# Kernel optimization log

Hardware: AMD Instinct MI355X
Metric: run time of the kernel (lower is better)

Reference implementation:

```python
import jax, jax.numpy as jnp
import numpy as np

N_HEAD = 16
ROT_DIM = 64  # head_dim * rotary_percentage(1.0)
ROPE_BASE = 10000.0
NEG_INF = -1.0e9


def _rope_cos_sin(seq_len, rd):
    # freqs: [S, rd//2]; original code builds cos/sin per pair; we repeat each
    # entry twice so it applies to the interleaved (even, odd) pair layout.
    inv_freq = 1.0 / (ROPE_BASE ** (jnp.arange(0, rd, 2, dtype=jnp.float32) / rd))
    freqs = jnp.arange(seq_len, dtype=jnp.float32)[:, None] * inv_freq[None, :]
    cos = jnp.repeat(jnp.cos(freqs), 2, axis=-1)  # [S, rd]
    sin = jnp.repeat(jnp.sin(freqs), 2, axis=-1)  # [S, rd]
    return cos, sin


def _rotate_pairs(x):
    # interleaved pairs: (x0, x1) -> (-x1, x0), matching apply_rotary_embeddings
    x2 = x.reshape(x.shape[:-1] + (-1, 2))
    r = jnp.stack([-x2[..., 1], x2[..., 0]], axis=-1)
    return r.reshape(x.shape)


def reference(x, W_attn, W_proj, cache_k, cache_v):
    B, S, D = x.shape
    H = N_HEAD
    HD = D // H
    # fused QKV projection (Linear, bias=False)
    qkv = x @ W_attn  # [B, S, 3D]
    q, k, v = jnp.split(qkv, 3, axis=-1)
    q = q.reshape(B, S, H, HD).transpose(0, 2, 1, 3)  # [B,H,S,HD]
    k = k.reshape(B, S, H, HD).transpose(0, 2, 1, 3)
    v = v.reshape(B, S, H, HD).transpose(0, 2, 1, 3)
    # rotary on first ROT_DIM dims; q = q*cos - rot(q)*sin (original sign conv.)
    cos, sin = _rope_cos_sin(S, ROT_DIM)  # [S, ROT_DIM] broadcasts over B,H
    q_r, q_p = q[..., :ROT_DIM], q[..., ROT_DIM:]
    k_r, k_p = k[..., :ROT_DIM], k[..., ROT_DIM:]
    q_r = q_r * cos - _rotate_pairs(q_r) * sin
    k_r = k_r * cos - _rotate_pairs(k_r) * sin
    q = jnp.concatenate([q_r, q_p], axis=-1)
    k = jnp.concatenate([k_r, k_p], axis=-1)
    # KV-cache write at past_length=0 (prefill), then read back full context
    k_full = jax.lax.dynamic_update_slice(cache_k, k, (0, 0, 0, 0))
    v_full = jax.lax.dynamic_update_slice(cache_v, v, (0, 0, 0, 0))
    T = k_full.shape[2]  # full_seq_len == S here
    # causal additive mask (upper triangular * -1e9), as in the kv_cache branch
    mask = jnp.triu(jnp.ones((T, T), dtype=jnp.float32), k=1) * NEG_INF
    q = q * (1.0 / np.sqrt(HD).astype(np.float32))
    scores = jnp.einsum('bhqd,bhkd->bhqk', q, k_full) + mask
    att = jax.nn.softmax(scores, axis=-1)
    y = jnp.einsum('bhqk,bhkd->bhqd', att, v_full)
    y = y.transpose(0, 2, 1, 3).reshape(B, S, D)
    return y @ W_proj


def setup_inputs() -> dict:
    key = jax.random.key(0)
    k1, k2, k3 = jax.random.split(key, 3)
    B, S, D, H = 2, 2048, 1024, 16
    HD = D // H
    x = jax.random.normal(k1, (B, S, D), dtype=jnp.float32)
    W_attn = jax.random.normal(k2, (D, 3 * D), dtype=jnp.float32) * 0.02
    W_proj = jax.random.normal(k3, (D, D), dtype=jnp.float32) * 0.02
    cache_k = jnp.zeros((B, H, S, HD), dtype=jnp.float32)
    cache_v = jnp.zeros((B, H, S, HD), dtype=jnp.float32)
    return {"x": x, "W_attn": W_attn, "W_proj": W_proj, "cache_k": cache_k, "cache_v": cache_v}
```

## Files before the change

### kernel.cpp

```cpp
#include <hip/hip_runtime.h>
#include <stdint.h>

#define S_LEN 2048
#define NHEAD 16
#define DMODEL 1024

typedef __attribute__((ext_vector_type(8))) short short8;
typedef __attribute__((ext_vector_type(8))) __bf16 bf16x8;
typedef __attribute__((ext_vector_type(4))) float f32x4;

__device__ __forceinline__ unsigned short f2b(float f) {
  unsigned int u = __float_as_uint(f);
  u += 0x7fffu + ((u >> 16) & 1u);
  return (unsigned short)(u >> 16);
}
__device__ __forceinline__ float b2f(unsigned short h) {
  return __uint_as_float(((unsigned int)h) << 16);
}
__device__ __forceinline__ f32x4 mfma16(short8 a, short8 b, f32x4 c) {
  return __builtin_amdgcn_mfma_f32_16x16x32_bf16(
      __builtin_bit_cast(bf16x8, a), __builtin_bit_cast(bf16x8, b), c, 0, 0, 0);
}
__device__ __forceinline__ void gload16(const void* g, void* l) {
  __builtin_amdgcn_global_load_lds(
      (const __attribute__((address_space(1))) unsigned int*)g,
      (__attribute__((address_space(3))) unsigned int*)l, 16, 0, 0);
}

__global__ __launch_bounds__(256) void cast_f32_bf16(
    const float* __restrict__ in, unsigned short* __restrict__ out, long n) {
  long i = ((long)blockIdx.x * 256 + threadIdx.x) * 4;
  if (i >= n) return;
  float4 v = *(const float4*)(in + i);
  ushort4 o;
  o.x = f2b(v.x); o.y = f2b(v.y); o.z = f2b(v.z); o.w = f2b(v.w);
  *(ushort4*)(out + i) = o;
}

__global__ __launch_bounds__(256) void transpose_cast(
    const float* __restrict__ W, unsigned short* __restrict__ Wt, int K, int N) {
  __shared__ float t[32][33];
  const int nt = blockIdx.x, kt = blockIdx.y;
  const int tx = threadIdx.x, ty = threadIdx.y;
#pragma unroll
  for (int j = 0; j < 4; ++j)
    t[ty + j * 8][tx] = W[(long)(kt * 32 + ty + j * 8) * N + nt * 32 + tx];
  __syncthreads();
#pragma unroll
  for (int j = 0; j < 4; ++j)
    Wt[(long)(nt * 32 + ty + j * 8) * K + kt * 32 + tx] = f2b(t[tx][ty + j * 8]);
}

__global__ __launch_bounds__(256) void make_tab(float2* __restrict__ tab) {
  int i = blockIdx.x * 256 + threadIdx.x;
  if (i >= S_LEN * 32) return;
  int s = i >> 5, fi = i & 31;
  float inv = powf(10000.0f, -(float)(2 * fi) / 64.0f);
  float fr = (float)s * inv;
  tab[i] = make_float2(cosf(fr), sinf(fr));
}

template <int OUT_BF16>
__global__ __launch_bounds__(256) void gemm_bt(
    const unsigned short* __restrict__ A, const unsigned short* __restrict__ Bt,
    void* __restrict__ Cout, int M, int N, int K) {
  __shared__ __align__(16) unsigned short As[128 * 32];
  __shared__ __align__(16) unsigned short Bs[128 * 32];
  const int tid = threadIdx.x;
  const int wave = tid >> 6, lane = tid & 63;
  const int g = lane >> 4, r15 = lane & 15;
  const int wm = wave >> 1, wn = wave & 1;
  const long m0 = (long)blockIdx.x * 128, n0 = (long)blockIdx.y * 128;
  const int srow = tid >> 2, scol = (tid & 3) * 8;
  const unsigned short* Ag = A + (m0 + srow) * K + scol;
  const unsigned short* Bg = Bt + (n0 + srow) * K + scol;
  unsigned short* As0 = &As[srow * 32 + scol];
  unsigned short* As1 = &As[(srow + 64) * 32 + scol];
  unsigned short* Bs0 = &Bs[srow * 32 + scol];
  unsigned short* Bs1 = &Bs[(srow + 64) * 32 + scol];
  f32x4 acc[4][4] = {};
  for (int kt = 0; kt < K; kt += 32) {
    __syncthreads();
    gload16(Ag + kt, As0);
    gload16(Ag + (long)64 * K + kt, As1);
    gload16(Bg + kt, Bs0);
    gload16(Bg + (long)64 * K + kt, Bs1);
    __syncthreads();
    short8 a[4], b[4];
#pragma unroll
    for (int m = 0; m < 4; ++m)
      a[m] = *(const short8*)&As[(wm * 64 + m * 16 + r15) * 32 + g * 8];
#pragma unroll
    for (int n = 0; n < 4; ++n)
      b[n] = *(const short8*)&Bs[(wn * 64 + n * 16 + r15) * 32 + g * 8];
#pragma unroll
    for (int m = 0; m < 4; ++m)
#pragma unroll
      for (int n = 0; n < 4; ++n)
        acc[m][n] = mfma16(a[m], b[n], acc[m][n]);
  }
#pragma unroll
  for (int m = 0; m < 4; ++m)
#pragma unroll
    for (int n = 0; n < 4; ++n)
#pragma unroll
      for (int r = 0; r < 4; ++r) {
        long row = m0 + wm * 64 + m * 16 + g * 4 + r;
        long col = n0 + wn * 64 + n * 16 + r15;
        if (OUT_BF16)
          ((unsigned short*)Cout)[row * N + col] = f2b(acc[m][n][r]);
        else
          ((float*)Cout)[row * N + col] = acc[m][n][r];
      }
}

__global__ __launch_bounds__(256) void rope_scatter(
    const unsigned short* __restrict__ qkv, const float2* __restrict__ tab,
    unsigned short* __restrict__ Qb, unsigned short* __restrict__ Kb) {
  long p = (long)blockIdx.x * 256 + threadIdx.x;
  if (p >= (long)4096 * 1024) return;
  int row = (int)(p >> 10);
  int col = ((int)(p & 1023)) * 2;
  int seg = col >> 10;
  int cc = col & 1023;
  int h = cc >> 6, d = cc & 63;
  int b = row >> 11, s = row & 2047;
  const unsigned short* src = qkv + (long)row * 3072 + col;
  float v0 = b2f(src[0]), v1 = b2f(src[1]);
  float2 f = tab[s * 32 + (d >> 1)];
  float o0 = v0 * f.x + v1 * f.y;
  float o1 = v1 * f.x - v0 * f.y;
  float scl = seg ? 1.0f : 0.125f;
  unsigned short* dst = (seg ? Kb : Qb) + (((long)(b * NHEAD + h) * S_LEN + s) * 64 + d);
  dst[0] = f2b(o0 * scl);
  dst[1] = f2b(o1 * scl);
}

__global__ __launch_bounds__(256) void v_transpose(
    const unsigned short* __restrict__ qkv, unsigned short* __restrict__ Vt) {
  __shared__ unsigned short t[64][33];
  const int st = blockIdx.x;
  const int dt = blockIdx.y;
  const int bh = blockIdx.z;
  const int b = bh >> 4, h = bh & 15;
  const int tx = threadIdx.x, ty = threadIdx.y;
#pragma unroll
  for (int j = 0; j < 8; ++j)
    t[ty + j * 8][tx] =
        qkv[((long)b * S_LEN + st * 64 + ty + j * 8) * 3072 + 2048 + h * 64 + dt * 32 + tx];
  __syncthreads();
#pragma unroll
  for (int j = 0; j < 4; ++j) {
    const int d_local = ty + j * 8;
#pragma unroll
    for (int jj = 0; jj < 2; ++jj) {
      const int col = jj * 32 + tx;
      const int kv = (col & 3) * 16 + (col >> 2);
      Vt[((long)bh * 64 + dt * 32 + d_local) * S_LEN + st * 64 + col] = t[kv][d_local];
    }
  }
}

__device__ __forceinline__ void load_k(const unsigned short* __restrict__ Kp,
                                       int kpos, int c, int g, short8 kf[4][2]) {
#pragma unroll
  for (int s = 0; s < 4; ++s)
#pragma unroll
    for (int hh = 0; hh < 2; ++hh)
      kf[s][hh] = *(const short8*)(Kp + (long)(kpos + s * 16 + c) * 64 + hh * 32 + g * 8);
}
__device__ __forceinline__ void load_v(const unsigned short* __restrict__ Vp,
                                       int kpos, int c, int g, short8 vf[4][2]) {
#pragma unroll
  for (int dt = 0; dt < 4; ++dt)
#pragma unroll
    for (int hh = 0; hh < 2; ++hh)
      vf[dt][hh] = *(const short8*)(Vp + (long)(dt * 16 + c) * S_LEN + kpos + hh * 32 + g * 8);
}

template <bool MASKED, bool PREFETCH>
__device__ __forceinline__ void attn_tile(
    int kpos0, int qbase, int c, int g,
    const short8& q0, const short8& q1,
    short8 kf[4][2], short8 vf[4][2],
    f32x4 O[4], float mrow[4], float lrow[4],
    unsigned char* PwB,
    const unsigned short* __restrict__ Kp, const unsigned short* __restrict__ Vp) {
  f32x4 s[4];
#pragma unroll
  for (int sub = 0; sub < 4; ++sub) {
    f32x4 z = {};
    z = mfma16(q0, kf[sub][0], z);
    s[sub] = mfma16(q1, kf[sub][1], z);
  }
  if (PREFETCH) load_k(Kp, kpos0 + 64, c, g, kf);
  float sc[4];
#pragma unroll
  for (int r = 0; r < 4; ++r) {
    float a0 = s[0][r], a1 = s[1][r], a2 = s[2][r], a3 = s[3][r];
    if (MASKED) {
      const int q = qbase + g * 4 + r;
      a0 = (kpos0 + c <= q) ? a0 : -1e30f;
      a1 = (kpos0 + 16 + c <= q) ? a1 : -1e30f;
      a2 = (kpos0 + 32 + c <= q) ? a2 : -1e30f;
      a3 = (kpos0 + 48 + c <= q) ? a3 : -1e30f;
    }
    float mt = fmaxf(fmaxf(a0, a1), fmaxf(a2, a3));
    mt = fmaxf(mt, __shfl_xor(mt, 1));
    mt = fmaxf(mt, __shfl_xor(mt, 2));
    mt = fmaxf(mt, __shfl_xor(mt, 4));
    mt = fmaxf(mt, __shfl_xor(mt, 8));
    const float mnew = fmaxf(mrow[r], mt);
    sc[r] = __expf(mrow[r] - mnew);
    mrow[r] = mnew;
    a0 = __expf(a0 - mnew);
    a1 = __expf(a1 - mnew);
    a2 = __expf(a2 - mnew);
    a3 = __expf(a3 - mnew);
    float rs = (a0 + a1) + (a2 + a3);
    rs += __shfl_xor(rs, 1);
    rs += __shfl_xor(rs, 2);
    rs += __shfl_xor(rs, 4);
    rs += __shfl_xor(rs, 8);
    lrow[r] = lrow[r] * sc[r] + rs;
    unsigned int lo, hi;
    asm("v_cvt_pk_bf16_f32 %0, %1, %2" : "=v"(lo) : "v"(a0), "v"(a1));
    asm("v_cvt_pk_bf16_f32 %0, %1, %2" : "=v"(hi) : "v"(a2), "v"(a3));
    const int qr = g * 4 + r;
    *(uint2*)(PwB + qr * 128 + ((c * 8) ^ ((qr & 7) << 4))) = make_uint2(lo, hi);
  }
#pragma unroll
  for (int dt = 0; dt < 4; ++dt) {
    f32x4 o = O[dt];
    o[0] *= sc[0]; o[1] *= sc[1]; o[2] *= sc[2]; o[3] *= sc[3];
    O[dt] = o;
  }
  __builtin_amdgcn_wave_barrier();
  const int rb = c * 128, swz = (c & 7) << 4;
  const short8 pa0 = *(const short8*)(PwB + rb + ((g * 16) ^ swz));
  const short8 pa1 = *(const short8*)(PwB + rb + ((64 + g * 16) ^ swz));
#pragma unroll
  for (int dt = 0; dt < 4; ++dt) {
    O[dt] = mfma16(pa0, vf[dt][0], O[dt]);
    O[dt] = mfma16(pa1, vf[dt][1], O[dt]);
  }
  __builtin_amdgcn_wave_barrier();
  if (PREFETCH) load_v(Vp, kpos0 + 64, c, g, vf);
}

__global__ __launch_bounds__(64) void attn_v3(
    const unsigned short* __restrict__ Qb, const unsigned short* __restrict__ Kb,
    const unsigned short* __restrict__ Vt, unsigned short* __restrict__ yb) {
  __shared__ __align__(16) unsigned char PwB[2048];
  const int flat = (int)blockIdx.x + ((int)blockIdx.y << 7);
  const int xcd = flat & 7;
  const int rest = flat >> 3;
  const int bh = xcd * 4 + (rest >> 7);
  const int p = 127 - (rest & 127);
  const int lane = (int)threadIdx.x & 63;
  const int g = lane >> 4, c = lane & 15;
  const int b = bh >> 4, h = bh & 15;
  const unsigned short* Kp = Kb + (long)bh * (S_LEN * 64);
  const unsigned short* Vp = Vt + (long)bh * (64 * S_LEN);
  short8 kf[4][2], vf[4][2];

  const int qbase = p << 4;
  const unsigned short* Qp = Qb + ((long)bh * S_LEN + qbase) * 64;
  const short8 q0 = *(const short8*)(Qp + c * 64 + g * 8);
  const short8 q1 = *(const short8*)(Qp + c * 64 + 32 + g * 8);
  f32x4 O[4] = {};
  float mrow[4] = {-1e30f, -1e30f, -1e30f, -1e30f};
  float lrow[4] = {0.f, 0.f, 0.f, 0.f};
  const int nfull = qbase >> 6;

  load_k(Kp, 0, c, g, kf);
  load_v(Vp, 0, c, g, vf);
  for (int t = 0; t < nfull; ++t)
    attn_tile<false, true>(t * 64, qbase, c, g, q0, q1, kf, vf, O, mrow, lrow, PwB, Kp, Vp);
  attn_tile<true, false>(nfull * 64, qbase, c, g, q0, q1, kf, vf, O, mrow, lrow, PwB, Kp, Vp);

  float inv[4];
#pragma unroll
  for (int r = 0; r < 4; ++r) inv[r] = 1.0f / lrow[r];
#pragma unroll
  for (int dt = 0; dt < 4; ++dt)
#pragma unroll
    for (int r = 0; r < 4; ++r) {
      long row = (long)b * S_LEN + qbase + g * 4 + r;
      yb[row * DMODEL + h * 64 + dt * 16 + c] = f2b(O[dt][r] * inv[r]);
    }
}

extern "C" void kernel_launch(void* const* d_in, const int* in_sizes, int n_in,
                              void* d_out, int out_size, void* d_ws, size_t ws_size,
                              hipStream_t stream) {
  const float* x = (const float*)d_in[0];
  const float* Wa = (const float*)d_in[1];
  const float* Wp = (const float*)d_in[2];
  float* out = (float*)d_out;

  char* ws = (char*)d_ws;
  size_t off = 0;
  auto alloc = [&](size_t bytes) -> void* {
    off = (off + 255) & ~(size_t)255;
    void* p = ws + off;
    off += bytes;
    return p;
  };
  unsigned short* xb   = (unsigned short*)alloc((size_t)4096 * 1024 * 2);
  unsigned short* WaT  = (unsigned short*)alloc((size_t)3072 * 1024 * 2);
  unsigned short* WpT  = (unsigned short*)alloc((size_t)1024 * 1024 * 2);
  unsigned short* qkvb = (unsigned short*)alloc((size_t)4096 * 3072 * 2);
  float2* tab          = (float2*)alloc((size_t)2048 * 32 * sizeof(float2));
  unsigned short* Qb   = (unsigned short*)alloc((size_t)32 * 2048 * 64 * 2);
  unsigned short* Kb   = (unsigned short*)alloc((size_t)32 * 2048 * 64 * 2);
  unsigned short* Vt   = (unsigned short*)alloc((size_t)32 * 2048 * 64 * 2);
  unsigned short* yb   = xb;

  dim3 tB(32, 8);
  cast_f32_bf16<<<4096, 256, 0, stream>>>(x, xb, (long)4096 * 1024);
  transpose_cast<<<dim3(96, 32), tB, 0, stream>>>(Wa, WaT, 1024, 3072);
  transpose_cast<<<dim3(32, 32), tB, 0, stream>>>(Wp, WpT, 1024, 1024);
  make_tab<<<256, 256, 0, stream>>>(tab);
  gemm_bt<1><<<dim3(32, 24), 256, 0, stream>>>(xb, WaT, (void*)qkvb, 4096, 3072, 1024);
  rope_scatter<<<16384, 256, 0, stream>>>(qkvb, tab, Qb, Kb);
  v_transpose<<<dim3(32, 2, 32), tB, 0, stream>>>(qkvb, Vt);
  attn_v3<<<dim3(128, 32), 64, 0, stream>>>(Qb, Kb, Vt, yb);
  gemm_bt<0><<<dim3(32, 8), 256, 0, stream>>>(yb, WpT, (void*)out, 4096, 1024, 1024);
}
```

Baseline: 317.0 us.

## Switch attention to 32x32x16 MFMA with transposed scores and register-only P

Rewrites the attention kernel to use 32x32x16 bf16 MFMA, computing S^T = K·Q^T so each lane owns one query row. Softmax row reductions then need only a single cross-half shuffle. P is passed to the PV MFMA through lane shuffles instead of a shared-memory round trip. Each wave now handles 32 queries instead of 16, so the grid halves and K/V loads are reused across more rows. The V transpose drops its interleaved permutation to match the new layout. The cost is a larger per-thread register footprint and fewer, heavier waves.

Measured after the change: 277.2 us. 1.14x faster.

```diff
diff --git a/kernel.cpp b/kernel.cpp
--- a/kernel.cpp
+++ b/kernel.cpp
@@ -8,6 +8,7 @@
 typedef __attribute__((ext_vector_type(8))) short short8;
 typedef __attribute__((ext_vector_type(8))) __bf16 bf16x8;
 typedef __attribute__((ext_vector_type(4))) float f32x4;
+typedef __attribute__((ext_vector_type(16))) float f32x16;
 
 __device__ __forceinline__ unsigned short f2b(float f) {
   unsigned int u = __float_as_uint(f);
@@ -20,6 +21,15 @@
 __device__ __forceinline__ f32x4 mfma16(short8 a, short8 b, f32x4 c) {
   return __builtin_amdgcn_mfma_f32_16x16x32_bf16(
       __builtin_bit_cast(bf16x8, a), __builtin_bit_cast(bf16x8, b), c, 0, 0, 0);
+}
+__device__ __forceinline__ f32x16 mfma32(short8 a, short8 b, f32x16 c) {
+  return __builtin_amdgcn_mfma_f32_32x32x16_bf16(
+      __builtin_bit_cast(bf16x8, a), __builtin_bit_cast(bf16x8, b), c, 0, 0, 0);
+}
+__device__ __forceinline__ unsigned int cvtpk(float lo, float hi) {
+  unsigned int r;
+  asm("v_cvt_pk_bf16_f32 %0, %1, %2" : "=v"(r) : "v"(lo), "v"(hi));
+  return r;
 }
 __device__ __forceinline__ void gload16(const void* g, void* l) {
   __builtin_amdgcn_global_load_lds(
@@ -155,139 +165,141 @@
 #pragma unroll
     for (int jj = 0; jj < 2; ++jj) {
       const int col = jj * 32 + tx;
-      const int kv = (col & 3) * 16 + (col >> 2);
-      Vt[((long)bh * 64 + dt * 32 + d_local) * S_LEN + st * 64 + col] = t[kv][d_local];
+      Vt[((long)bh * 64 + dt * 32 + d_local) * S_LEN + st * 64 + col] = t[col][d_local];
     }
   }
 }
 
-__device__ __forceinline__ void load_k(const unsigned short* __restrict__ Kp,
-                                       int kpos, int c, int g, short8 kf[4][2]) {
-#pragma unroll
-  for (int s = 0; s < 4; ++s)
-#pragma unroll
-    for (int hh = 0; hh < 2; ++hh)
-      kf[s][hh] = *(const short8*)(Kp + (long)(kpos + s * 16 + c) * 64 + hh * 32 + g * 8);
-}
-__device__ __forceinline__ void load_v(const unsigned short* __restrict__ Vp,
-                                       int kpos, int c, int g, short8 vf[4][2]) {
-#pragma unroll
-  for (int dt = 0; dt < 4; ++dt)
-#pragma unroll
-    for (int hh = 0; hh < 2; ++hh)
-      vf[dt][hh] = *(const short8*)(Vp + (long)(dt * 16 + c) * S_LEN + kpos + hh * 32 + g * 8);
+__device__ __forceinline__ void load_k32(const unsigned short* __restrict__ Kp,
+                                         int kv0, int q31, int hi, short8 kf[2][4]) {
+#pragma unroll
+  for (int sub = 0; sub < 2; ++sub)
+#pragma unroll
+    for (int dc = 0; dc < 4; ++dc)
+      kf[sub][dc] = *(const short8*)(Kp + (long)(kv0 + sub * 32 + q31) * 64 + dc * 16 + hi * 8);
+}
+__device__ __forceinline__ void load_v32(const unsigned short* __restrict__ Vp,
+                                         int kv0, int q31, int hi, short8 vf[2][4]) {
+#pragma unroll
+  for (int dv = 0; dv < 2; ++dv)
+#pragma unroll
+    for (int c = 0; c < 4; ++c)
+      vf[dv][c] = *(const short8*)(Vp + (long)(dv * 32 + q31) * S_LEN + kv0 + c * 16 + hi * 8);
 }
 
 template <bool MASKED, bool PREFETCH>
-__device__ __forceinline__ void attn_tile(
-    int kpos0, int qbase, int c, int g,
-    const short8& q0, const short8& q1,
-    short8 kf[4][2], short8 vf[4][2],
-    f32x4 O[4], float mrow[4], float lrow[4],
-    unsigned char* PwB,
+__device__ __forceinline__ void attn_tile32(
+    int kv0, int qbase, int q31, int hi,
+    const short8 qf[4], short8 kf[2][4], short8 vf[2][4],
+    f32x16& o0, f32x16& o1, float& m, float& l,
     const unsigned short* __restrict__ Kp, const unsigned short* __restrict__ Vp) {
-  f32x4 s[4];
-#pragma unroll
-  for (int sub = 0; sub < 4; ++sub) {
-    f32x4 z = {};
-    z = mfma16(q0, kf[sub][0], z);
-    s[sub] = mfma16(q1, kf[sub][1], z);
-  }
-  if (PREFETCH) load_k(Kp, kpos0 + 64, c, g, kf);
-  float sc[4];
-#pragma unroll
-  for (int r = 0; r < 4; ++r) {
-    float a0 = s[0][r], a1 = s[1][r], a2 = s[2][r], a3 = s[3][r];
-    if (MASKED) {
-      const int q = qbase + g * 4 + r;
-      a0 = (kpos0 + c <= q) ? a0 : -1e30f;
-      a1 = (kpos0 + 16 + c <= q) ? a1 : -1e30f;
-      a2 = (kpos0 + 32 + c <= q) ? a2 : -1e30f;
-      a3 = (kpos0 + 48 + c <= q) ? a3 : -1e30f;
+  f32x16 s0 = {}, s1 = {};
+#pragma unroll
+  for (int dc = 0; dc < 4; ++dc) s0 = mfma32(kf[0][dc], qf[dc], s0);
+#pragma unroll
+  for (int dc = 0; dc < 4; ++dc) s1 = mfma32(kf[1][dc], qf[dc], s1);
+  if (PREFETCH) load_k32(Kp, kv0 + 64, q31, hi, kf);
+  if (MASKED) {
+    const int q = qbase + q31;
+#pragma unroll
+    for (int i = 0; i < 16; ++i) {
+      const int rel = (i & 3) + 8 * (i >> 2) + 4 * hi;
+      s0[i] = (kv0 + rel <= q) ? s0[i] : -1e30f;
+      s1[i] = (kv0 + 32 + rel <= q) ? s1[i] : -1e30f;
     }
-    float mt = fmaxf(fmaxf(a0, a1), fmaxf(a2, a3));
-    mt = fmaxf(mt, __shfl_xor(mt, 1));
-    mt = fmaxf(mt, __shfl_xor(mt, 2));
-    mt = fmaxf(mt, __shfl_xor(mt, 4));
-    mt = fmaxf(mt, __shfl_xor(mt, 8));
-    const float mnew = fmaxf(mrow[r], mt);
-    sc[r] = __expf(mrow[r] - mnew);
-    mrow[r] = mnew;
-    a0 = __expf(a0 - mnew);
-    a1 = __expf(a1 - mnew);
-    a2 = __expf(a2 - mnew);
-    a3 = __expf(a3 - mnew);
-    float rs = (a0 + a1) + (a2 + a3);
-    rs += __shfl_xor(rs, 1);
-    rs += __shfl_xor(rs, 2);
-    rs += __shfl_xor(rs, 4);
-    rs += __shfl_xor(rs, 8);
-    lrow[r] = lrow[r] * sc[r] + rs;
-    unsigned int lo, hi;
-    asm("v_cvt_pk_bf16_f32 %0, %1, %2" : "=v"(lo) : "v"(a0), "v"(a1));
-    asm("v_cvt_pk_bf16_f32 %0, %1, %2" : "=v"(hi) : "v"(a2), "v"(a3));
-    const int qr = g * 4 + r;
-    *(uint2*)(PwB + qr * 128 + ((c * 8) ^ ((qr & 7) << 4))) = make_uint2(lo, hi);
-  }
-#pragma unroll
-  for (int dt = 0; dt < 4; ++dt) {
-    f32x4 o = O[dt];
-    o[0] *= sc[0]; o[1] *= sc[1]; o[2] *= sc[2]; o[3] *= sc[3];
-    O[dt] = o;
-  }
-  __builtin_amdgcn_wave_barrier();
-  const int rb = c * 128, swz = (c & 7) << 4;
-  const short8 pa0 = *(const short8*)(PwB + rb + ((g * 16) ^ swz));
-  const short8 pa1 = *(const short8*)(PwB + rb + ((64 + g * 16) ^ swz));
-#pragma unroll
-  for (int dt = 0; dt < 4; ++dt) {
-    O[dt] = mfma16(pa0, vf[dt][0], O[dt]);
-    O[dt] = mfma16(pa1, vf[dt][1], O[dt]);
-  }
-  __builtin_amdgcn_wave_barrier();
-  if (PREFETCH) load_v(Vp, kpos0 + 64, c, g, vf);
-}
-
-__global__ __launch_bounds__(64) void attn_v3(
+  }
+  float t8[8];
+#pragma unroll
+  for (int i = 0; i < 8; ++i)
+    t8[i] = fmaxf(fmaxf(s0[2 * i], s0[2 * i + 1]), fmaxf(s1[2 * i], s1[2 * i + 1]));
+  float mt = fmaxf(fmaxf(fmaxf(t8[0], t8[1]), fmaxf(t8[2], t8[3])),
+                   fmaxf(fmaxf(t8[4], t8[5]), fmaxf(t8[6], t8[7])));
+  mt = fmaxf(mt, __shfl_xor(mt, 32));
+  const float mnew = fmaxf(m, mt);
+  const float scl = __expf(m - mnew);
+  m = mnew;
+#pragma unroll
+  for (int i = 0; i < 16; ++i) {
+    s0[i] = __expf(s0[i] - mnew);
+    s1[i] = __expf(s1[i] - mnew);
+  }
+  float a8[8];
+#pragma unroll
+  for (int i = 0; i < 8; ++i)
+    a8[i] = (s0[2 * i] + s0[2 * i + 1]) + (s1[2 * i] + s1[2 * i + 1]);
+  float rs = ((a8[0] + a8[1]) + (a8[2] + a8[3])) + ((a8[4] + a8[5]) + (a8[6] + a8[7]));
+  rs += __shfl_xor(rs, 32);
+  l = l * scl + rs;
+#pragma unroll
+  for (int i = 0; i < 16; ++i) { o0[i] *= scl; o1[i] *= scl; }
+#pragma unroll
+  for (int c = 0; c < 4; ++c) {
+    const int rb = (c & 1) * 8;
+    float v0, v1, v2, v3, v4, v5, v6, v7;
+    if (c < 2) {
+      v0 = s0[rb + 0]; v1 = s0[rb + 1]; v2 = s0[rb + 2]; v3 = s0[rb + 3];
+      v4 = s0[rb + 4]; v5 = s0[rb + 5]; v6 = s0[rb + 6]; v7 = s0[rb + 7];
+    } else {
+      v0 = s1[rb + 0]; v1 = s1[rb + 1]; v2 = s1[rb + 2]; v3 = s1[rb + 3];
+      v4 = s1[rb + 4]; v5 = s1[rb + 5]; v6 = s1[rb + 6]; v7 = s1[rb + 7];
+    }
+    const unsigned int wa = cvtpk(v0, v1), wb = cvtpk(v2, v3);
+    const unsigned int wc = cvtpk(v4, v5), wd = cvtpk(v6, v7);
+    const unsigned int sa = (unsigned int)__shfl_xor((int)wa, 32);
+    const unsigned int sb = (unsigned int)__shfl_xor((int)wb, 32);
+    const unsigned int sc_ = (unsigned int)__shfl_xor((int)wc, 32);
+    const unsigned int sd = (unsigned int)__shfl_xor((int)wd, 32);
+    uint4 pw = hi ? make_uint4(sc_, sd, wc, wd) : make_uint4(wa, wb, sa, sb);
+    const short8 pf = __builtin_bit_cast(short8, pw);
+    o0 = mfma32(vf[0][c], pf, o0);
+    o1 = mfma32(vf[1][c], pf, o1);
+  }
+  if (PREFETCH) load_v32(Vp, kv0 + 64, q31, hi, vf);
+}
+
+__global__ __launch_bounds__(64) void attn_v4(
     const unsigned short* __restrict__ Qb, const unsigned short* __restrict__ Kb,
     const unsigned short* __restrict__ Vt, unsigned short* __restrict__ yb) {
-  __shared__ __align__(16) unsigned char PwB[2048];
-  const int flat = (int)blockIdx.x + ((int)blockIdx.y << 7);
+  const int flat = (int)blockIdx.x + ((int)blockIdx.y << 6);
   const int xcd = flat & 7;
   const int rest = flat >> 3;
-  const int bh = xcd * 4 + (rest >> 7);
-  const int p = 127 - (rest & 127);
+  const int bh = xcd * 4 + (rest >> 6);
+  const int qt = 63 - (rest & 63);
   const int lane = (int)threadIdx.x & 63;
-  const int g = lane >> 4, c = lane & 15;
+  const int q31 = lane & 31, hi = lane >> 5;
   const int b = bh >> 4, h = bh & 15;
+  const int qbase = qt * 32;
   const unsigned short* Kp = Kb + (long)bh * (S_LEN * 64);
   const unsigned short* Vp = Vt + (long)bh * (64 * S_LEN);
-  short8 kf[4][2], vf[4][2];
-
-  const int qbase = p << 4;
   const unsigned short* Qp = Qb + ((long)bh * S_LEN + qbase) * 64;
-  const short8 q0 = *(const short8*)(Qp + c * 64 + g * 8);
-  const short8 q1 = *(const short8*)(Qp + c * 64 + 32 + g * 8);
-  f32x4 O[4] = {};
-  float mrow[4] = {-1e30f, -1e30f, -1e30f, -1e30f};
-  float lrow[4] = {0.f, 0.f, 0.f, 0.f};
+  short8 qf[4];
+#pragma unroll
+  for (int dc = 0; dc < 4; ++dc)
+    qf[dc] = *(const short8*)(Qp + q31 * 64 + dc * 16 + hi * 8);
+  short8 kf[2][4], vf[2][4];
+  f32x16 o0 = {}, o1 = {};
+  float m = -1e30f, l = 0.f;
   const int nfull = qbase >> 6;
 
-  load_k(Kp, 0, c, g, kf);
-  load_v(Vp, 0, c, g, vf);
+  load_k32(Kp, 0, q31, hi, kf);
+  load_v32(Vp, 0, q31, hi, vf);
   for (int t = 0; t < nfull; ++t)
-    attn_tile<false, true>(t * 64, qbase, c, g, q0, q1, kf, vf, O, mrow, lrow, PwB, Kp, Vp);
-  attn_tile<true, false>(nfull * 64, qbase, c, g, q0, q1, kf, vf, O, mrow, lrow, PwB, Kp, Vp);
-
-  float inv[4];
-#pragma unroll
-  for (int r = 0; r < 4; ++r) inv[r] = 1.0f / lrow[r];
-#pragma unroll
-  for (int dt = 0; dt < 4; ++dt)
-#pragma unroll
-    for (int r = 0; r < 4; ++r) {
-      long row = (long)b * S_LEN + qbase + g * 4 + r;
-      yb[row * DMODEL + h * 64 + dt * 16 + c] = f2b(O[dt][r] * inv[r]);
+    attn_tile32<false, true>(t * 64, qbase, q31, hi, qf, kf, vf, o0, o1, m, l, Kp, Vp);
+  attn_tile32<true, false>(nfull * 64, qbase, q31, hi, qf, kf, vf, o0, o1, m, l, Kp, Vp);
+
+  const float inv = 1.0f / l;
+  unsigned short* yrow = yb + ((long)b * S_LEN + qbase + q31) * DMODEL + h * 64;
+#pragma unroll
+  for (int a2 = 0; a2 < 2; ++a2)
+#pragma unroll
+    for (int q2 = 0; q2 < 4; ++q2) {
+      float e0, e1, e2, e3;
+      if (a2 == 0) { e0 = o0[q2 * 4]; e1 = o0[q2 * 4 + 1]; e2 = o0[q2 * 4 + 2]; e3 = o0[q2 * 4 + 3]; }
+      else         { e0 = o1[q2 * 4]; e1 = o1[q2 * 4 + 1]; e2 = o1[q2 * 4 + 2]; e3 = o1[q2 * 4 + 3]; }
+      uint2 w;
+      w.x = cvtpk(e0 * inv, e1 * inv);
+      w.y = cvtpk(e2 * inv, e3 * inv);
+      *(uint2*)(yrow + a2 * 32 + q2 * 8 + hi * 4) = w;
     }
 }
 
@@ -325,6 +337,6 @@
   gemm_bt<1><<<dim3(32, 24), 256, 0, stream>>>(xb, WaT, (void*)qkvb, 4096, 3072, 1024);
   rope_scatter<<<16384, 256, 0, stream>>>(qkvb, tab, Qb, Kb);
   v_transpose<<<dim3(32, 2, 32), tB, 0, stream>>>(qkvb, Vt);
-  attn_v3<<<dim3(128, 32), 64, 0, stream>>>(Qb, Kb, Vt, yb);
+  attn_v4<<<dim3(64, 32), 64, 0, stream>>>(Qb, Kb, Vt, yb);
   gemm_bt<0><<<dim3(32, 8), 256, 0, stream>>>(yb, WpT, (void*)out, 4096, 1024, 1024);
 }
```
